# Kernel optimization log

Measured on AMD Instinct MI355X. Metric: run time of the kernel, lower is better.

## Reference

```python
import jax, jax.numpy as jnp
import numpy as np

DIM = 1024
HEADS = 16
HEAD_DIM = DIM // HEADS


def setup_inputs() -> dict:
    key = jax.random.key(0)
    ks = jax.random.split(key, 10)
    B, N, M = 4, 2048, 2048
    s = 1.0 / np.sqrt(DIM)
    return {
        "x": jax.random.normal(ks[0], (B, N, DIM), jnp.float32),
        "context": jax.random.normal(ks[1], (B, M, DIM), jnp.float32),
        "Wq": jax.random.normal(ks[2], (DIM, DIM), jnp.float32) * s,
        "bq": jnp.zeros((DIM,), jnp.float32),
        "Wk": jax.random.normal(ks[3], (DIM, DIM), jnp.float32) * s,
        "bk": jnp.zeros((DIM,), jnp.float32),
        "Wv": jax.random.normal(ks[4], (DIM, DIM), jnp.float32) * s,
        "bv": jnp.zeros((DIM,), jnp.float32),
        "Wo": jax.random.normal(ks[5], (DIM, DIM), jnp.float32) * s,
        "bo": jnp.zeros((DIM,), jnp.float32),
    }


def reference(x, context, Wq, bq, Wk, bk, Wv, bv, Wo, bo):
    B, N, C = x.shape
    M = context.shape[1]
    scale = HEAD_DIM ** (-0.5)
    # projections + split heads: [B, H, L, D]
    q = (x @ Wq.T + bq).reshape(B, N, HEADS, HEAD_DIM).transpose(0, 2, 1, 3)
    k = (context @ Wk.T + bk).reshape(B, M, HEADS, HEAD_DIM).transpose(0, 2, 1, 3)
    v = (context @ Wv.T + bv).reshape(B, M, HEADS, HEAD_DIM).transpose(0, 2, 1, 3)
    attn = jax.nn.softmax(jnp.einsum('bhnd,bhmd->bhnm', q, k) * scale, axis=-1)
    out = jnp.einsum('bhnm,bhmd->bhnd', attn, v)  # [B, H, N, D]
    out = out.transpose(0, 2, 1, 3).reshape(B, N, C)
    return out @ Wo.T + bo
```

## Files before the change

### kernel.cpp

```cpp
#include <hip/hip_runtime.h>
#include <hip/hip_bf16.h>
#include <stdint.h>


#define HEADS 16
#define HD 64
#define NSEQ 2048
#define DIMSZ 1024

typedef __bf16 bf16x8_t __attribute__((ext_vector_type(8)));
typedef float f32x4_t __attribute__((ext_vector_type(4)));
typedef short s16x4 __attribute__((ext_vector_type(4)));
typedef unsigned short u16;
typedef unsigned int u32;

__device__ __forceinline__ u16 f2bf(float f) {
    union { float f; u32 i; } x; x.f = f;
    u32 r = x.i + 0x7FFF + ((x.i >> 16) & 1);
    return (u16)(r >> 16);
}
__device__ __forceinline__ u32 pk2(float a, float b) {
    __hip_bfloat162 h = __float22bfloat162_rn(float2{a, b});
    union { __hip_bfloat162 h2; u32 u; } c; c.h2 = h; return c.u;
}

__device__ __forceinline__ void pl32swap(u32& a, u32& b) {
    asm("v_permlane32_swap_b32 %0, %1" : "+v"(a), "+v"(b));
}
__device__ __forceinline__ void pl16swap(u32& a, u32& b) {
    asm("v_permlane16_swap_b32 %0, %1" : "+v"(a), "+v"(b));
}

#define GLDS(g, l) __builtin_amdgcn_global_load_lds( \
    (const __attribute__((address_space(1))) void*)(g), \
    (__attribute__((address_space(3))) void*)(l), 16, 0, 0)

__global__ __launch_bounds__(256)
void cvt_all(const float* __restrict__ x, const float* __restrict__ ctx,
             const float* __restrict__ wq, const float* __restrict__ wk,
             const float* __restrict__ wv, const float* __restrict__ wo,
             u16* __restrict__ xb, u16* __restrict__ ctxb,
             u16* __restrict__ wqb, u16* __restrict__ wkb,
             u16* __restrict__ wvb, u16* __restrict__ wob)
{
    long g = (long)blockIdx.x * 256 + threadIdx.x;
    const float* in; u16* out; long off;
    if (g < 1048576L)      { in = x;   out = xb;   off = g; }
    else if (g < 2097152L) { in = ctx; out = ctxb; off = g - 1048576L; }
    else if (g < 2228224L) { in = wq;  out = wqb;  off = g - 2097152L; }
    else if (g < 2359296L) { in = wk;  out = wkb;  off = g - 2228224L; }
    else if (g < 2490368L) { in = wv;  out = wvb;  off = g - 2359296L; }
    else                   { in = wo;  out = wob;  off = g - 2490368L; }
    long i = off * 8;
    float4 a = *(const float4*)(in + i);
    float4 b = *(const float4*)(in + i + 4);
    union { uint4 v; u16 h[8]; } u;
    u.h[0] = f2bf(a.x); u.h[1] = f2bf(a.y); u.h[2] = f2bf(a.z); u.h[3] = f2bf(a.w);
    u.h[4] = f2bf(b.x); u.h[5] = f2bf(b.y); u.h[6] = f2bf(b.z); u.h[7] = f2bf(b.w);
    *(uint4*)(out + i) = u.v;
}

#define BM 128
#define BN 128

#define BKQ 64

__global__ __launch_bounds__(256, 3)
void qkv_gemm(const u16* __restrict__ xb, const u16* __restrict__ ctxb,
              const u16* __restrict__ wq, const u16* __restrict__ wk,
              const u16* __restrict__ wv,
              const float* __restrict__ bq, const float* __restrict__ bk,
              const float* __restrict__ bv,
              u16* __restrict__ qo, u16* __restrict__ ko, u16* __restrict__ vo,
              float qscale)
{
    __shared__ __align__(16) u16 Asm[BM * BKQ];
    __shared__ __align__(16) u16 Wsm[BN * BKQ];

    const int g    = blockIdx.x >> 3;
    const int col0 = (blockIdx.x & 7) * BN;
    const int row0 = blockIdx.y * BM;

    const u16* A = (g == 0) ? xb : ctxb;
    const u16* W = (g == 0) ? wq : (g == 1) ? wk : wv;
    const float* bias = (g == 0) ? bq : (g == 1) ? bk : bv;
    const float scale = (g == 0) ? qscale : 1.0f;

    const int t    = threadIdx.x;
    const int lane = t & 63;
    const int wid  = t >> 6;
    const int lrow = lane & 15;
    const int lq   = lane >> 4;
    const int wm   = (wid >> 1) * 64;
    const int wn   = (wid & 1) * 64;

    const u16* gA[4]; const u16* gW[4];
    u16* lA[4]; u16* lW[4];
    #pragma unroll
    for (int q = 0; q < 4; q++) {
        int s = q * 256 + t;
        int r = s >> 3;
        int c = (s & 7) ^ (r & 7);
        gA[q] = A + (long)(row0 + r) * DIMSZ + c * 8;
        gW[q] = W + (long)(col0 + r) * DIMSZ + c * 8;
        int lofs = (q * 256 + wid * 64) * 8;
        lA[q] = &Asm[lofs];
        lW[q] = &Wsm[lofs];
    }

    f32x4_t zero = {0.f, 0.f, 0.f, 0.f};
    f32x4_t acc[4][4];
    #pragma unroll
    for (int i = 0; i < 4; i++)
        #pragma unroll
        for (int j = 0; j < 4; j++) acc[i][j] = zero;

    const int rsw = lrow & 7;

    for (int k0 = 0; k0 < DIMSZ; k0 += BKQ) {
        __syncthreads();
        #pragma unroll
        for (int q = 0; q < 4; q++) {
            GLDS(gA[q] + k0, lA[q]);
            GLDS(gW[q] + k0, lW[q]);
        }
        __syncthreads();

        #pragma unroll
        for (int kk = 0; kk < 2; kk++) {
            bf16x8_t af[4], bfr[4];
            #pragma unroll
            for (int i = 0; i < 4; i++)
                af[i] = *(const bf16x8_t*)
                    &Asm[(wm + 16 * i + lrow) * BKQ + (((kk * 4 + lq) ^ rsw) << 3)];
            #pragma unroll
            for (int j = 0; j < 4; j++)
                bfr[j] = *(const bf16x8_t*)
                    &Wsm[(wn + 16 * j + lrow) * BKQ + (((kk * 4 + lq) ^ rsw) << 3)];
            #pragma unroll
            for (int i = 0; i < 4; i++)
                #pragma unroll
                for (int j = 0; j < 4; j++)
                    acc[i][j] = __builtin_amdgcn_mfma_f32_16x16x32_bf16(
                        af[i], bfr[j], acc[i][j], 0, 0, 0);
        }
    }

    float bvv[4];
    #pragma unroll
    for (int j = 0; j < 4; j++) bvv[j] = bias[col0 + wn + 16 * j + lrow];

    if (g < 2) {
        u16* out = g ? ko : qo;
        #pragma unroll
        for (int i = 0; i < 4; i++) {
            #pragma unroll
            for (int j = 0; j < 4; j++) {
                int cc = col0 + wn + 16 * j + lrow;
                #pragma unroll
                for (int r = 0; r < 4; r++) {
                    int rr = row0 + wm + 16 * i + lq * 4 + r;
                    float v = (acc[i][j][r] + bvv[j]) * scale;
                    int b = rr >> 11, n = rr & 2047;
                    int h = cc >> 6,  d = cc & 63;
                    long oidx = ((long)((b * HEADS + h) * NSEQ + n) << 6) + d;
                    out[oidx] = f2bf(v);
                }
            }
        }
    } else {
        #pragma unroll
        for (int i = 0; i < 4; i++) {
            int n0 = row0 + wm + 16 * i + lq * 4;
            int b  = n0 >> 11, nn = n0 & 2047;
            #pragma unroll
            for (int j = 0; j < 4; j++) {
                int d = col0 + wn + 16 * j + lrow;
                uint2 p;
                p.x = pk2(acc[i][j][0] + bvv[j], acc[i][j][1] + bvv[j]);
                p.y = pk2(acc[i][j][2] + bvv[j], acc[i][j][3] + bvv[j]);
                long o = ((long)((b * HEADS + (d >> 6)) * HD + (d & 63)) << 11) + nn;
                *(uint2*)&vo[o] = p;
            }
        }
    }
}

#define BMO 64
#define BKO 64

__global__ __launch_bounds__(256, 4)
void gemm_o(const u16* __restrict__ A, const u16* __restrict__ W,
            const float* __restrict__ bias, float* __restrict__ out)
{
    __shared__ __align__(16) u16 Asm[BMO * BKO];
    __shared__ __align__(16) u16 Wsm[BN * BKO];

    const int t    = threadIdx.x;
    const int lane = t & 63;
    const int wid  = t >> 6;
    const int lrow = lane & 15;
    const int lq   = lane >> 4;
    const int wm   = (wid >> 1) * 32;
    const int wn   = (wid & 1) * 64;
    const int row0 = blockIdx.y * BMO;
    const int col0 = blockIdx.x * BN;

    const u16* gA[2]; u16* lA[2];
    #pragma unroll
    for (int q = 0; q < 2; q++) {
        int s = q * 256 + t;
        int r = s >> 3;
        int c = (s & 7) ^ (r & 7);
        gA[q] = A + (long)(row0 + r) * DIMSZ + c * 8;
        lA[q] = &Asm[(q * 256 + wid * 64) * 8];
    }
    const u16* gW[4]; u16* lW[4];
    #pragma unroll
    for (int q = 0; q < 4; q++) {
        int s = q * 256 + t;
        int r = s >> 3;
        int c = (s & 7) ^ (r & 7);
        gW[q] = W + (long)(col0 + r) * DIMSZ + c * 8;
        lW[q] = &Wsm[(q * 256 + wid * 64) * 8];
    }

    f32x4_t zero = {0.f, 0.f, 0.f, 0.f};
    f32x4_t acc[2][4];
    #pragma unroll
    for (int i = 0; i < 2; i++)
        #pragma unroll
        for (int j = 0; j < 4; j++) acc[i][j] = zero;

    const int rsw = lrow & 7;

    for (int k0 = 0; k0 < DIMSZ; k0 += BKO) {
        __syncthreads();
        GLDS(gA[0] + k0, lA[0]);
        GLDS(gA[1] + k0, lA[1]);
        #pragma unroll
        for (int q = 0; q < 4; q++) GLDS(gW[q] + k0, lW[q]);
        __syncthreads();

        #pragma unroll
        for (int kk = 0; kk < 2; kk++) {
            bf16x8_t af[2], bfr[4];
            #pragma unroll
            for (int i = 0; i < 2; i++)
                af[i] = *(const bf16x8_t*)
                    &Asm[(wm + 16 * i + lrow) * BKO + (((kk * 4 + lq) ^ rsw) << 3)];
            #pragma unroll
            for (int j = 0; j < 4; j++)
                bfr[j] = *(const bf16x8_t*)
                    &Wsm[(wn + 16 * j + lrow) * BKO + (((kk * 4 + lq) ^ rsw) << 3)];
            #pragma unroll
            for (int i = 0; i < 2; i++)
                #pragma unroll
                for (int j = 0; j < 4; j++)
                    acc[i][j] = __builtin_amdgcn_mfma_f32_16x16x32_bf16(
                        af[i], bfr[j], acc[i][j], 0, 0, 0);
        }
    }

    float bvv[4];
    #pragma unroll
    for (int j = 0; j < 4; j++) bvv[j] = bias[col0 + wn + 16 * j + lrow];

    #pragma unroll
    for (int i = 0; i < 2; i++) {
        #pragma unroll
        for (int j = 0; j < 4; j++) {
            int cc = col0 + wn + 16 * j + lrow;
            #pragma unroll
            for (int r = 0; r < 4; r++) {
                int rr = row0 + wm + 16 * i + lq * 4 + r;
                out[(long)rr * DIMSZ + cc] = acc[i][j][r] + bvv[j];
            }
        }
    }
}

__global__ __launch_bounds__(256, 4)
void attn(const u16* __restrict__ Q, const u16* __restrict__ K,
          const u16* __restrict__ Vt, u16* __restrict__ O)
{
    __shared__ __align__(16) u16 Ksm[64 * 64];
    __shared__ __align__(16) u16 Vsm[64 * 64];

    const int t    = threadIdx.x;
    const int lane = t & 63;
    const int w    = t >> 6;
    const int lrow = lane & 15;
    const int lq   = lane >> 4;
    const int bh   = blockIdx.x;
    const int q0   = blockIdx.y * 128;
    const int b    = bh >> 4;
    const int h    = bh & 15;

    bf16x8_t qf[2][2];
    #pragma unroll
    for (int qa = 0; qa < 2; qa++) {
        const long qbase = ((long)bh * NSEQ + q0 + w * 32 + qa * 16 + lrow) * HD;
        qf[qa][0] = *(const bf16x8_t*)&Q[qbase + lq * 8];
        qf[qa][1] = *(const bf16x8_t*)&Q[qbase + lq * 8 + 32];
    }

    const long kvbase = (long)bh * NSEQ * HD;

    const u16* gK[2]; const u16* gV[2]; u16* lK[2]; u16* lV[2];
    #pragma unroll
    for (int c = 0; c < 2; c++) {
        int s  = c * 256 + t;
        int r  = s >> 3;
        int ch = (s & 7) ^ (r & 7);
        gK[c] = K  + kvbase + (long)r * HD + ch * 8;
        gV[c] = Vt + kvbase + (long)r * NSEQ + ch * 8;
        int lofs = (c * 256 + w * 64) * 8;
        lK[c] = &Ksm[lofs];
        lV[c] = &Vsm[lofs];
    }

    f32x4_t zero = {0.f, 0.f, 0.f, 0.f};
    f32x4_t oacc[2][4];
    #pragma unroll
    for (int qa = 0; qa < 2; qa++)
        #pragma unroll
        for (int jd = 0; jd < 4; jd++) oacc[qa][jd] = zero;
    float lsum[2] = {0.f, 0.f};

    const int rsw = lrow & 7;

    for (int kt = 0; kt < NSEQ / 64; kt++) {
        __syncthreads();
        GLDS(gK[0] + (long)kt * 64 * HD, lK[0]);
        GLDS(gK[1] + (long)kt * 64 * HD, lK[1]);
        GLDS(gV[0] + kt * 64, lV[0]);
        GLDS(gV[1] + kt * 64, lV[1]);
        __syncthreads();

        f32x4_t sacc[2][4];
        #pragma unroll
        for (int jt = 0; jt < 4; jt++) {
            sacc[0][jt] = zero; sacc[1][jt] = zero;
            #pragma unroll
            for (int kk = 0; kk < 2; kk++) {
                bf16x8_t kf = *(const bf16x8_t*)
                    &Ksm[(16 * jt + lrow) * 64 + (((kk * 4 + lq) ^ rsw) << 3)];
                sacc[0][jt] = __builtin_amdgcn_mfma_f32_16x16x32_bf16(
                    kf, qf[0][kk], sacc[0][jt], 0, 0, 0);
                sacc[1][jt] = __builtin_amdgcn_mfma_f32_16x16x32_bf16(
                    kf, qf[1][kk], sacc[1][jt], 0, 0, 0);
            }
        }

        bf16x8_t pa32[2][2];
        #pragma unroll
        for (int qa = 0; qa < 2; qa++) {
            #pragma unroll
            for (int t2 = 0; t2 < 2; t2++) {
                u32 uu[2][2];
                #pragma unroll
                for (int half = 0; half < 2; half++) {
                    int jt = t2 * 2 + half;
                    float p0 = exp2f(sacc[qa][jt][0]);
                    float p1 = exp2f(sacc[qa][jt][1]);
                    float p2 = exp2f(sacc[qa][jt][2]);
                    float p3 = exp2f(sacc[qa][jt][3]);
                    lsum[qa] += (p0 + p1) + (p2 + p3);
                    uu[half][0] = pk2(p0, p1);
                    uu[half][1] = pk2(p2, p3);
                }
                pl32swap(uu[0][0], uu[1][0]);
                pl16swap(uu[0][0], uu[1][0]);
                pl32swap(uu[0][1], uu[1][1]);
                pl16swap(uu[0][1], uu[1][1]);
                union { u32 u[4]; bf16x8_t v; } pk_;
                pk_.u[0] = uu[0][0]; pk_.u[1] = uu[0][1];
                pk_.u[2] = uu[1][0]; pk_.u[3] = uu[1][1];
                pa32[qa][t2] = pk_.v;
            }
        }

        #pragma unroll
        for (int jd = 0; jd < 4; jd++) {
            #pragma unroll
            for (int t2 = 0; t2 < 2; t2++) {
                bf16x8_t vb = *(const bf16x8_t*)
                    &Vsm[(16 * jd + lrow) * 64 + (((4 * t2 + lq) ^ rsw) << 3)];
                oacc[0][jd] = __builtin_amdgcn_mfma_f32_16x16x32_bf16(
                    pa32[0][t2], vb, oacc[0][jd], 0, 0, 0);
                oacc[1][jd] = __builtin_amdgcn_mfma_f32_16x16x32_bf16(
                    pa32[1][t2], vb, oacc[1][jd], 0, 0, 0);
            }
        }
    }

    float linv[2][4];
    #pragma unroll
    for (int qa = 0; qa < 2; qa++) {
        lsum[qa] += __shfl_xor(lsum[qa], 16, 64);
        lsum[qa] += __shfl_xor(lsum[qa], 32, 64);
        #pragma unroll
        for (int r = 0; r < 4; r++)
            linv[qa][r] = __builtin_amdgcn_rcpf(__shfl(lsum[qa], lq * 4 + r, 64));
    }

    #pragma unroll
    for (int qa = 0; qa < 2; qa++) {
        #pragma unroll
        for (int jd = 0; jd < 4; jd++) {
            #pragma unroll
            for (int r = 0; r < 4; r++) {
                int qrow = q0 + w * 32 + qa * 16 + lq * 4 + r;
                int d    = 16 * jd + lrow;
                long oidx = ((long)(b * NSEQ + qrow)) * DIMSZ + h * HD + d;
                O[oidx] = f2bf(oacc[qa][jd][r] * linv[qa][r]);
            }
        }
    }
}

extern "C" void kernel_launch(void* const* d_in, const int* in_sizes, int n_in,
                              void* d_out, int out_size, void* d_ws, size_t ws_size,
                              hipStream_t stream)
{
    const float* x   = (const float*)d_in[0];
    const float* ctx = (const float*)d_in[1];
    const float* Wq  = (const float*)d_in[2];
    const float* bq  = (const float*)d_in[3];
    const float* Wk  = (const float*)d_in[4];
    const float* bk  = (const float*)d_in[5];
    const float* Wv  = (const float*)d_in[6];
    const float* bv  = (const float*)d_in[7];
    const float* Wo  = (const float*)d_in[8];
    const float* bo  = (const float*)d_in[9];
    float* out = (float*)d_out;

    const size_t NX = (size_t)8192 * 1024;
    const size_t NW = (size_t)1024 * 1024;

    u16* xb   = (u16*)d_ws;
    u16* ctxb = xb + NX;
    u16* wqb  = ctxb + NX;
    u16* wkb  = wqb + NW;
    u16* wvb  = wkb + NW;
    u16* wob  = wvb + NW;
    u16* qws  = wob + NW;
    u16* kws  = qws + NX;
    u16* vws  = kws + NX;
    u16* aws  = xb;

    cvt_all<<<10240, 256, 0, stream>>>(x, ctx, Wq, Wk, Wv, Wo,
                                       xb, ctxb, wqb, wkb, wvb, wob);

    const float qscale = 0.125f * 1.44269504088896340736f;

    qkv_gemm<<<dim3(24, 8192 / BM), 256, 0, stream>>>(
        xb, ctxb, wqb, wkb, wvb, bq, bk, bv, qws, kws, vws, qscale);
    attn<<<dim3(64, NSEQ / 128), 256, 0, stream>>>(qws, kws, vws, aws);
    gemm_o<<<dim3(DIMSZ / BN, 8192 / BMO), 256, 0, stream>>>(aws, wob, bo, out);
}
```

Baseline: 359.4 us.

## Double-buffer K/V tiles in attention and compute row sums via MFMA

The attention kernel now keeps two LDS buffers for K and V. It issues the global-to-LDS load for the next tile before computing the current one, so memory transfer overlaps with MFMA and exp work and one barrier per tile is dropped. The scalar per-lane accumulation of softmax denominators is replaced by an extra MFMA against a ones vector, which also removes the cross-lane shuffles at the end. The cost is doubled LDS use (32 KB per block), which may limit occupancy at 4 blocks per CU, plus extra MFMA issue and a row sum taken over bf16-rounded probabilities.

New measurement: 342.5 us. 4.7% less time.

```diff
diff --git a/kernel.cpp b/kernel.cpp
--- a/kernel.cpp
+++ b/kernel.cpp
@@ -284,8 +284,8 @@
 void attn(const u16* __restrict__ Q, const u16* __restrict__ K,
           const u16* __restrict__ Vt, u16* __restrict__ O)
 {
-    __shared__ __align__(16) u16 Ksm[64 * 64];
-    __shared__ __align__(16) u16 Vsm[64 * 64];
+    __shared__ __align__(16) u16 Ksm[2][64 * 64];
+    __shared__ __align__(16) u16 Vsm[2][64 * 64];
 
     const int t    = threadIdx.x;
     const int lane = t & 63;
@@ -307,7 +307,7 @@
 
     const long kvbase = (long)bh * NSEQ * HD;
 
-    const u16* gK[2]; const u16* gV[2]; u16* lK[2]; u16* lV[2];
+    const u16* gK[2]; const u16* gV[2]; int lofs[2];
     #pragma unroll
     for (int c = 0; c < 2; c++) {
         int s  = c * 256 + t;
@@ -315,9 +315,7 @@
         int ch = (s & 7) ^ (r & 7);
         gK[c] = K  + kvbase + (long)r * HD + ch * 8;
         gV[c] = Vt + kvbase + (long)r * NSEQ + ch * 8;
-        int lofs = (c * 256 + w * 64) * 8;
-        lK[c] = &Ksm[lofs];
-        lV[c] = &Vsm[lofs];
+        lofs[c] = (c * 256 + w * 64) * 8;
     }
 
     f32x4_t zero = {0.f, 0.f, 0.f, 0.f};
@@ -326,18 +324,24 @@
     for (int qa = 0; qa < 2; qa++)
         #pragma unroll
         for (int jd = 0; jd < 4; jd++) oacc[qa][jd] = zero;
-    float lsum[2] = {0.f, 0.f};
+    f32x4_t lacc[2] = {zero, zero};
+
+    union { u32 u[4]; bf16x8_t v; } ob;
+    ob.u[0] = ob.u[1] = ob.u[2] = ob.u[3] = 0x3F803F80u;
+    const bf16x8_t onesb = ob.v;
 
     const int rsw = lrow & 7;
 
-    for (int kt = 0; kt < NSEQ / 64; kt++) {
-        __syncthreads();
-        GLDS(gK[0] + (long)kt * 64 * HD, lK[0]);
-        GLDS(gK[1] + (long)kt * 64 * HD, lK[1]);
-        GLDS(gV[0] + kt * 64, lV[0]);
-        GLDS(gV[1] + kt * 64, lV[1]);
-        __syncthreads();
-
+    auto stage = [&](int ktn, int nb) {
+        long ko = (long)ktn * (64 * HD);
+        int  vo = ktn * 64;
+        GLDS(gK[0] + ko, &Ksm[nb][lofs[0]]);
+        GLDS(gK[1] + ko, &Ksm[nb][lofs[1]]);
+        GLDS(gV[0] + vo, &Vsm[nb][lofs[0]]);
+        GLDS(gV[1] + vo, &Vsm[nb][lofs[1]]);
+    };
+
+    auto tile = [&](const u16* Ks, const u16* Vs) {
         f32x4_t sacc[2][4];
         #pragma unroll
         for (int jt = 0; jt < 4; jt++) {
@@ -345,7 +349,7 @@
             #pragma unroll
             for (int kk = 0; kk < 2; kk++) {
                 bf16x8_t kf = *(const bf16x8_t*)
-                    &Ksm[(16 * jt + lrow) * 64 + (((kk * 4 + lq) ^ rsw) << 3)];
+                    &Ks[(16 * jt + lrow) * 64 + (((kk * 4 + lq) ^ rsw) << 3)];
                 sacc[0][jt] = __builtin_amdgcn_mfma_f32_16x16x32_bf16(
                     kf, qf[0][kk], sacc[0][jt], 0, 0, 0);
                 sacc[1][jt] = __builtin_amdgcn_mfma_f32_16x16x32_bf16(
@@ -366,7 +370,6 @@
                     float p1 = exp2f(sacc[qa][jt][1]);
                     float p2 = exp2f(sacc[qa][jt][2]);
                     float p3 = exp2f(sacc[qa][jt][3]);
-                    lsum[qa] += (p0 + p1) + (p2 + p3);
                     uu[half][0] = pk2(p0, p1);
                     uu[half][1] = pk2(p2, p3);
                 }
@@ -378,6 +381,8 @@
                 pk_.u[0] = uu[0][0]; pk_.u[1] = uu[0][1];
                 pk_.u[2] = uu[1][0]; pk_.u[3] = uu[1][1];
                 pa32[qa][t2] = pk_.v;
+                lacc[qa] = __builtin_amdgcn_mfma_f32_16x16x32_bf16(
+                    pa32[qa][t2], onesb, lacc[qa], 0, 0, 0);
             }
         }
 
@@ -386,24 +391,33 @@
             #pragma unroll
             for (int t2 = 0; t2 < 2; t2++) {
                 bf16x8_t vb = *(const bf16x8_t*)
-                    &Vsm[(16 * jd + lrow) * 64 + (((4 * t2 + lq) ^ rsw) << 3)];
+                    &Vs[(16 * jd + lrow) * 64 + (((4 * t2 + lq) ^ rsw) << 3)];
                 oacc[0][jd] = __builtin_amdgcn_mfma_f32_16x16x32_bf16(
                     pa32[0][t2], vb, oacc[0][jd], 0, 0, 0);
                 oacc[1][jd] = __builtin_amdgcn_mfma_f32_16x16x32_bf16(
                     pa32[1][t2], vb, oacc[1][jd], 0, 0, 0);
             }
         }
+    };
+
+    stage(0, 0);
+    __syncthreads();
+
+    for (int kt = 0; kt < NSEQ / 64; kt += 2) {
+        stage(kt + 1, 1);
+        tile(Ksm[0], Vsm[0]);
+        __syncthreads();
+        if (kt + 2 < NSEQ / 64) stage(kt + 2, 0);
+        tile(Ksm[1], Vsm[1]);
+        __syncthreads();
     }
 
     float linv[2][4];
     #pragma unroll
-    for (int qa = 0; qa < 2; qa++) {
-        lsum[qa] += __shfl_xor(lsum[qa], 16, 64);
-        lsum[qa] += __shfl_xor(lsum[qa], 32, 64);
+    for (int qa = 0; qa < 2; qa++)
         #pragma unroll
         for (int r = 0; r < 4; r++)
-            linv[qa][r] = __builtin_amdgcn_rcpf(__shfl(lsum[qa], lq * 4 + r, 64));
-    }
+            linv[qa][r] = __builtin_amdgcn_rcpf(lacc[qa][r]);
 
     #pragma unroll
     for (int qa = 0; qa < 2; qa++) {
```
